# Optimization experiments

Measured on AMD Instinct MI355X. Metric: run time of the kernel, lower is better.

## Reference

```python
import jax, jax.numpy as jnp
import numpy as np

EPS = 1e-6
SINKHORN_ITERS = 8
TEMPERATURE = 1.0
B, N, D = 4, 8192, 512
E, OUT = 8, 512
H = 1


def setup_inputs() -> dict:
    key = jax.random.key(0)
    k1, k2, k3 = jax.random.split(key, 3)
    x = jax.random.normal(k1, (B, N, D), dtype=jnp.float32)
    gate_weight = jax.random.normal(k2, (H, D, E), dtype=jnp.float32)
    experts = jax.random.normal(k3, (E, D, OUT), dtype=jnp.float32) * 0.02
    return {"x": x, "gate_weight": gate_weight, "experts": experts}


def _sinkhorn(logits):
    # logits: (b, h, n, e). log(clamp(.,eps)) then alternating row/col log-normalization.
    t = jnp.log(jnp.clip(logits, EPS)) / TEMPERATURE
    for _ in range(SINKHORN_ITERS):
        t = t - jax.nn.logsumexp(t, axis=-2, keepdims=True)  # normalize over tokens n
        t = t - jax.nn.logsumexp(t, axis=-1, keepdims=True)  # normalize over experts e
    return jnp.exp(t)


def reference(x, gate_weight, experts):
    b, n, d = x.shape
    e = experts.shape[0]
    m = n // e  # tokens per expert
    xh = x[:, None, :, :]  # b 1 n d  (single-headed -> h=1)
    gate_logits = jnp.einsum('bhnd,hde->bhne', xh, gate_weight)
    gates = _sinkhorn(gate_logits)  # b h n e
    # topk over token dim n, per expert: move n to last axis for lax.top_k
    g_t = jnp.swapaxes(gates, -1, -2)  # b h e n
    vals, idx = jax.lax.top_k(g_t, m)  # (b h e m), (b h e m)
    gate_values = jnp.transpose(vals, (2, 0, 1, 3))[..., None]  # e b h m 1
    # gather routed tokens: routed[e,b,h,m,d] = x[b,h,idx[b,h,e,m],d]
    routed = jnp.take_along_axis(xh[:, :, None, :, :], idx[..., None], axis=3)  # b h e m d
    routed = jnp.transpose(routed, (2, 0, 1, 3, 4))  # e b h m d
    expert_w = experts[:, None, :, :]  # e h i o with h=1 (rearrange 'e i o -> e 1 i o')
    outputs = jnp.einsum('ebhmi,ehio->ebhmo', routed, expert_w)  # e b h m o
    outputs = outputs * gate_values
    # scatter back (set semantics, matching einx set_at)
    bh_idx = idx.reshape(b, 1, e * m)  # b h (e m)
    bh_vals = jnp.transpose(outputs, (1, 2, 0, 3, 4)).reshape(b, 1, e * m, outputs.shape[-1])
    def scat(i1, v1):
        return jnp.zeros((n, v1.shape[-1]), dtype=v1.dtype).at[i1].set(v1)
    routed_back = jax.vmap(jax.vmap(scat))(bh_idx, bh_vals)  # b h n o
    return routed_back[:, 0]  # b n o
```

## Files before the change

kernel.cpp:

```cpp
#include <hip/hip_runtime.h>
#include <hip/hip_bf16.h>

#define BB 4
#define NN 8192
#define DD 512
#define EE 8
#define OUTD 512
#define TOPM 1024
#define EPSV 1e-6f
#define ITERS 8

using s16x8 = __attribute__((ext_vector_type(8))) short;
using f32x4 = __attribute__((ext_vector_type(4))) float;
typedef unsigned long long u64;

__device__ __forceinline__ unsigned short f2bf(float f) {
  unsigned u = __float_as_uint(f);
  return (unsigned short)((u + 0x7FFFu + ((u >> 16) & 1u)) >> 16);
}

__device__ __forceinline__ void gll16(const void* g, void* l) {
  __builtin_amdgcn_global_load_lds((const __attribute__((address_space(1))) void*)g,
                                   (__attribute__((address_space(3))) void*)l, 16, 0, 0);
}

__global__ __launch_bounds__(256) void k_gate(const float* __restrict__ x,
                                              const float* __restrict__ gw,
                                              float* __restrict__ t0,
                                              unsigned short* __restrict__ xbf,
                                              int* __restrict__ eo,
                                              int* __restrict__ counts,
                                              const float* __restrict__ W,
                                              unsigned short* __restrict__ WT) {
  const int tid = threadIdx.x;
  if (blockIdx.x >= 2048) {
    __shared__ float tl[32][33];
    const int widx = blockIdx.x - 2048;
    const int e = widx >> 8, rem = widx & 255;
    const int k0 = (rem >> 4) * 32, n0 = (rem & 15) * 32;
    const int ty = tid >> 5, tx = tid & 31;
    const float* src = W + ((long)e * DD + k0) * OUTD + n0;
#pragma unroll
    for (int j = 0; j < 4; ++j)
      tl[ty + j * 8][tx] = src[(long)(ty + j * 8) * OUTD + tx];
    __syncthreads();
    unsigned short* dst = WT + ((long)e * OUTD + n0) * DD + k0;
#pragma unroll
    for (int j = 0; j < 4; ++j)
      dst[(long)(ty + j * 8) * DD + tx] = f2bf(tl[tx][ty + j * 8]);
    return;
  }
  if (tid < 16) eo[blockIdx.x * 16 + tid] = -1;
  if (blockIdx.x == 0 && tid >= 64 && tid < 64 + BB * EE) counts[tid - 64] = 0;
  const int lane = tid & 63;
  const int w    = tid >> 6;
  float gwf[64];
  const float* gb = gw + (lane * 8) * EE;
#pragma unroll
  for (int q = 0; q < 16; ++q) {
    float4 t = *(const float4*)(gb + q * 4);
    gwf[q * 4 + 0] = t.x; gwf[q * 4 + 1] = t.y;
    gwf[q * 4 + 2] = t.z; gwf[q * 4 + 3] = t.w;
  }
#pragma unroll
  for (int q = 0; q < 64; ++q) asm volatile("" : "+v"(gwf[q]));

  const long row0 = (long)blockIdx.x * 16 + w * 4;
  float4 xa[4], xb[4];
#pragma unroll
  for (int i = 0; i < 4; ++i) {
    const float* xr = x + (row0 + i) * DD + lane * 8;
    xa[i] = *(const float4*)(xr);
    xb[i] = *(const float4*)(xr + 4);
  }
  float vout[4];
#pragma unroll
  for (int i = 0; i < 4; ++i) {
    float xv[8] = {xa[i].x, xa[i].y, xa[i].z, xa[i].w,
                   xb[i].x, xb[i].y, xb[i].z, xb[i].w};
    s16x8 xo;
#pragma unroll
    for (int j = 0; j < 8; ++j) xo[j] = (short)f2bf(xv[j]);
    *(s16x8*)(xbf + (row0 + i) * DD + lane * 8) = xo;

    float acc[8] = {0.f,0.f,0.f,0.f,0.f,0.f,0.f,0.f};
#pragma unroll
    for (int q = 0; q < 8; ++q)
#pragma unroll
      for (int e = 0; e < 8; ++e) acc[e] += xv[q] * gwf[q * 8 + e];
    const bool o1 = lane & 1;
    float own, oth, b0, b1, b2, b3, c0, c1, v;
    own = o1 ? acc[1] : acc[0]; oth = o1 ? acc[0] : acc[1];
    b0 = own + __shfl_xor(oth, 1);
    own = o1 ? acc[3] : acc[2]; oth = o1 ? acc[2] : acc[3];
    b1 = own + __shfl_xor(oth, 1);
    own = o1 ? acc[5] : acc[4]; oth = o1 ? acc[4] : acc[5];
    b2 = own + __shfl_xor(oth, 1);
    own = o1 ? acc[7] : acc[6]; oth = o1 ? acc[6] : acc[7];
    b3 = own + __shfl_xor(oth, 1);
    const bool o2 = lane & 2;
    own = o2 ? b1 : b0; oth = o2 ? b0 : b1;
    c0 = own + __shfl_xor(oth, 2);
    own = o2 ? b3 : b2; oth = o2 ? b2 : b3;
    c1 = own + __shfl_xor(oth, 2);
    const bool o4 = lane & 4;
    own = o4 ? c1 : c0; oth = o4 ? c0 : c1;
    v = own + __shfl_xor(oth, 4);
    v += __shfl_xor(v, 8);
    v += __shfl_xor(v, 16);
    v += __shfl_xor(v, 32);
    vout[i] = v;
  }
  const int gsel = lane >> 3;
  float vsel = vout[0];
  vsel = (gsel == 1) ? vout[1] : vsel;
  vsel = (gsel == 2) ? vout[2] : vsel;
  vsel = (gsel == 3) ? vout[3] : vsel;
  if (lane < 32) t0[row0 * EE + lane] = logf(fmaxf(vsel, EPSV));
}

__global__ __launch_bounds__(1024) void k_sink5(const float* __restrict__ t0,
                                                float* __restrict__ R,
                                                float* __restrict__ C) {
  const int b = blockIdx.x;
  const int tid = threadIdx.x;
  const int wv = tid >> 6, ln = tid & 63;
  const float* tb = t0 + (long)b * NN * EE;
  float E[8][8], u[8], dl[8];
  __shared__ float ws[16][8];
  __shared__ float Csh[8];
  __shared__ float Ssh[8];
#pragma unroll
  for (int j = 0; j < 8; ++j) {
    const float* p = tb + (long)(j * 1024 + tid) * EE;
    float4 a = *(const float4*)p, b4 = *(const float4*)(p + 4);
    E[j][0] = expf(a.x);  E[j][1] = expf(a.y);
    E[j][2] = expf(a.z);  E[j][3] = expf(a.w);
    E[j][4] = expf(b4.x); E[j][5] = expf(b4.y);
    E[j][6] = expf(b4.z); E[j][7] = expf(b4.w);
    u[j] = 1.f;
  }
  for (int it = 0; it < ITERS; ++it) {
    float P[8] = {0.f,0.f,0.f,0.f,0.f,0.f,0.f,0.f};
#pragma unroll
    for (int j = 0; j < 8; ++j)
#pragma unroll
      for (int e = 0; e < 8; ++e) P[e] += E[j][e] * u[j];
#pragma unroll
    for (int d = 1; d <= 4; d <<= 1) {
#pragma unroll
      for (int e = 0; e < 8; ++e) {
        float tmp = __shfl_xor(P[e], d);
        P[e] += ((ln & d) == (e & d)) ? tmp : 0.f;
      }
    }
    float pv = P[0];
#pragma unroll
    for (int e = 1; e < 8; ++e) pv = ((ln & 7) == e) ? P[e] : pv;
#pragma unroll
    for (int d = 8; d < 64; d <<= 1) pv += __shfl_xor(pv, d);
    if (ln < 8) ws[wv][ln] = pv;
    __syncthreads();
    if (tid < 64) {
      const int q = ln >> 3, e = ln & 7;
      float s = ws[q][e] + ws[q + 8][e];
#pragma unroll
      for (int d = 8; d < 64; d <<= 1) s += __shfl_xor(s, d);
      if (ln < 8) { Csh[ln] = 1.f / s; Ssh[ln] = s; }
    }
    __syncthreads();
    float vv[8];
#pragma unroll
    for (int e = 0; e < 8; ++e) vv[e] = Csh[e];
#pragma unroll
    for (int j = 0; j < 8; ++j) {
      float d0 = E[j][0] * vv[0];
#pragma unroll
      for (int e = 1; e < 8; ++e) d0 += E[j][e] * vv[e];
      dl[j] = d0;
      u[j] = 1.f / d0;
    }
    __syncthreads();
  }
#pragma unroll
  for (int j = 0; j < 8; ++j) R[(long)b * NN + j * 1024 + tid] = logf(dl[j]);
  if (tid < 8) C[b * EE + tid] = logf(Ssh[tid]);
}

__global__ __launch_bounds__(1024) void k_topk(const float* __restrict__ t0,
                                               const float* __restrict__ R,
                                               int* __restrict__ expert_of) {
  __shared__ unsigned key[NN];
  __shared__ int hist[256];
  __shared__ int bcast[2];
  __shared__ int wsum[16];
  const int b = blockIdx.x >> 3, e = blockIdx.x & 7;
  const int tid = threadIdx.x;
  const int wv = tid >> 6, ln = tid & 63;
  const float* t = t0 + (long)b * NN * EE + e;
  const float* Rb = R + b * NN;
  if (tid < 256) hist[tid] = 0;
  __syncthreads();
  for (int n = tid; n < NN; n += 1024) {
    float f = t[n * EE] - Rb[n];
    unsigned u = __float_as_uint(f);
    u = (u & 0x80000000u) ? ~u : (u | 0x80000000u);
    key[n] = u;
    atomicAdd(&hist[u >> 24], 1);
  }
  __syncthreads();
  unsigned prefix = 0, mask = 0;
  int k = TOPM;
  for (int shift = 24; shift >= 0; shift -= 8) {
    if (tid < 64) {
      const int4 h4 = *(const int4*)&hist[ln * 4];
      const int r3 = h4.w, r2 = h4.z + r3, r1 = h4.y + r2, r0 = h4.x + r1;
      int suf = r0;
#pragma unroll
      for (int d = 1; d < 64; d <<= 1) {
        int o = __shfl_down(suf, d);
        if (ln + d < 64) suf += o;
      }
      const int above = suf - r0;
      const int cum0 = above + r0, cum1 = above + r1;
      const int cum2 = above + r2, cum3 = above + r3;
      if (cum0 >= k && cum1 < k) { bcast[0] = k - cum1; bcast[1] = ln * 4 + 0; }
      if (cum1 >= k && cum2 < k) { bcast[0] = k - cum2; bcast[1] = ln * 4 + 1; }
      if (cum2 >= k && cum3 < k) { bcast[0] = k - cum3; bcast[1] = ln * 4 + 2; }
      if (cum3 >= k && above < k) { bcast[0] = k - above; bcast[1] = ln * 4 + 3; }
    }
    __syncthreads();
    k = bcast[0];
    prefix |= ((unsigned)bcast[1]) << shift;
    mask |= (255u << shift);
    if (shift == 0) break;
    if (tid < 256) hist[tid] = 0;
    __syncthreads();
    const int nsh = shift - 8;
    for (int n = tid; n < NN; n += 1024) {
      unsigned u = key[n];
      if ((u & mask) == prefix) atomicAdd(&hist[(u >> nsh) & 255], 1);
    }
    __syncthreads();
  }
  const unsigned theta = prefix;
  const int need = k;
  const int base = tid * 8;
  int c = 0;
#pragma unroll
  for (int j = 0; j < 8; ++j) if (key[base + j] == theta) ++c;
  int inc = c;
#pragma unroll
  for (int d = 1; d < 64; d <<= 1) {
    int o = __shfl_up(inc, d);
    if (ln >= d) inc += o;
  }
  if (ln == 63) wsum[wv] = inc;
  __syncthreads();
  if (tid == 0) {
    int runv = 0;
    for (int i = 0; i < 16; ++i) { int t2 = wsum[i]; wsum[i] = runv; runv += t2; }
  }
  __syncthreads();
  int run = wsum[wv] + inc - c;
  int* eo = expert_of + b * NN;
  for (int j = 0; j < 8; ++j) {
    int n = base + j;
    unsigned u = key[n];
    bool sel = false;
    if (u > theta) sel = true;
    else if (u == theta) { if (run < need) sel = true; ++run; }
    if (sel) atomicMax(&eo[n], e);
  }
}

__global__ __launch_bounds__(256) void k_post(const int* __restrict__ expert_of,
                                              const float* __restrict__ t0,
                                              const float* __restrict__ R,
                                              const float* __restrict__ C,
                                              int* __restrict__ counts,
                                              int* __restrict__ lists,
                                              float* __restrict__ gvals,
                                              float* __restrict__ out) {
  const int tid = threadIdx.x;
  if (blockIdx.x >= 128) {
    const int row = (blockIdx.x - 128) * 4 + (tid >> 6);
    if (expert_of[row] >= 0) return;
    const int ln = tid & 63;
    float4 z = make_float4(0.f, 0.f, 0.f, 0.f);
    float4* p = (float4*)(out + (long)row * OUTD) + ln;
    p[0] = z; p[64] = z;
    return;
  }
  __shared__ int hist8[8], base8[8];
  if (tid < 8) hist8[tid] = 0;
  __syncthreads();
  const long i = (long)blockIdx.x * 256 + tid;
  const int b = (int)(i >> 13);
  const int e = expert_of[i];
  int lpos = -1;
  if (e >= 0) lpos = atomicAdd(&hist8[e], 1);
  __syncthreads();
  if (tid < 8 && hist8[tid] > 0)
    base8[tid] = atomicAdd(&counts[b * EE + tid], hist8[tid]);
  __syncthreads();
  if (e >= 0) {
    const int n = (int)(i & (NN - 1));
    const int be = b * EE + e;
    const int slot = be * TOPM + base8[e] + lpos;
    lists[slot] = n;
    gvals[slot] = expf(t0[i * EE + e] - C[be] - R[i]);
  }
}

__global__ __launch_bounds__(256) void k_gemm(const unsigned short* __restrict__ xbf,
                                              const unsigned short* __restrict__ WT,
                                              const int* __restrict__ counts,
                                              const int* __restrict__ lists,
                                              const float* __restrict__ gvals,
                                              float* __restrict__ out) {
  const int id = blockIdx.x;
  const int xq = id >> 8;
  const int be = (id >> 3) & 31;
  const int yq = id & 7;
  const int b = be >> 3, e = be & 7;
  const int cnt = counts[be];
  const int r0 = yq * 128;
  if (r0 >= cnt) return;
  const int c0 = xq * 128;

  __shared__ unsigned short As[128 * 64];
  __shared__ unsigned short Bs[128 * 64];
  __shared__ int   rowTok[128];
  __shared__ float rowG[128];

  const int tid = threadIdx.x;
  if (tid < 128) {
    int r = r0 + tid;
    rowTok[tid] = (r < cnt) ? lists[be * TOPM + r] : -1;
    rowG[tid]   = (r < cnt) ? gvals[be * TOPM + r] : 0.f;
  }
  __syncthreads();

  const int w = tid >> 6, l = tid & 63;
  const int rbase = w * 32 + (l >> 3);
  const int sL = l & 7;
  const unsigned short* xb_b = xbf + (long)b * NN * DD;
  const unsigned short* wt_e = WT + (long)e * OUTD * DD;
  int tokc[4]; int sGa[4], sGb[4];
#pragma unroll
  for (int c = 0; c < 4; ++c) {
    int r = rbase + c * 8;
    int tk = rowTok[r]; if (tk < 0) tk = 0;
    tokc[c] = tk;
    sGa[c] = (sL ^ (r & 7)) * 8;
    sGb[c] = sGa[c];
  }

  const int wr = w >> 1, wc = w & 1;
  const int fr = l & 15, fq = l >> 4;
  int aoff[4][2], boff[4][2];
#pragma unroll
  for (int m = 0; m < 4; ++m) {
#pragma unroll
    for (int kk = 0; kk < 2; ++kk) {
      int row = wr * 64 + m * 16 + fr;
      aoff[m][kk] = row * 64 + (((fq + 4 * kk) ^ (row & 7)) * 8);
      int col = wc * 64 + m * 16 + fr;
      boff[m][kk] = col * 64 + (((fq + 4 * kk) ^ (col & 7)) * 8);
    }
  }

  f32x4 acc[4][4] = {};

#define STAGE(kb) {                                                          \
    int ko = (kb) * 64;                                                      \
    _Pragma("unroll")                                                        \
    for (int c = 0; c < 4; ++c) {                                            \
      int r = rbase + c * 8;                                                 \
      gll16(xb_b + (long)tokc[c] * DD + ko + sGa[c],                         \
            As + (w * 32 + c * 8) * 64);                                     \
      gll16(wt_e + (long)(c0 + r) * DD + ko + sGb[c],                        \
            Bs + (w * 32 + c * 8) * 64);                                     \
    }                                                                        \
  }

  STAGE(0);
  for (int kb = 0; kb < 8; ++kb) {
    __syncthreads();
    s16x8 af[4][2], bf_[4][2];
#pragma unroll
    for (int m = 0; m < 4; ++m) {
      af[m][0] = *(const s16x8*)(As + aoff[m][0]);
      af[m][1] = *(const s16x8*)(As + aoff[m][1]);
      bf_[m][0] = *(const s16x8*)(Bs + boff[m][0]);
      bf_[m][1] = *(const s16x8*)(Bs + boff[m][1]);
    }
    __syncthreads();
    if (kb < 7) STAGE(kb + 1);
#pragma unroll
    for (int kk = 0; kk < 2; ++kk)
#pragma unroll
      for (int m = 0; m < 4; ++m)
#pragma unroll
        for (int n = 0; n < 4; ++n)
          acc[m][n] = __builtin_amdgcn_mfma_f32_16x16x32_bf16(af[m][kk], bf_[n][kk], acc[m][n], 0, 0, 0);
  }
#undef STAGE

#pragma unroll
  for (int m = 0; m < 4; ++m) {
    int rbase2 = wr * 64 + m * 16 + fq * 4;
    int tok[4]; float g[4];
#pragma unroll
    for (int j = 0; j < 4; ++j) { tok[j] = rowTok[rbase2 + j]; g[j] = rowG[rbase2 + j]; }
#pragma unroll
    for (int n = 0; n < 4; ++n) {
      int col = c0 + wc * 64 + n * 16 + fr;
#pragma unroll
      for (int j = 0; j < 4; ++j) {
        if (tok[j] >= 0)
          out[((long)b * NN + tok[j]) * OUTD + col] = acc[m][n][j] * g[j];
      }
    }
  }
}

extern "C" void kernel_launch(void* const* d_in, const int* in_sizes, int n_in,
                              void* d_out, int out_size, void* d_ws, size_t ws_size,
                              hipStream_t stream) {
  const float* x  = (const float*)d_in[0];
  const float* gw = (const float*)d_in[1];
  const float* ex = (const float*)d_in[2];
  float* out = (float*)d_out;

  char* wsb = (char*)d_ws;
  float*          t0     = (float*)(wsb);
  unsigned short* xbf    = (unsigned short*)(wsb + (1l << 20));
  unsigned short* WT     = (unsigned short*)(wsb + (33l << 20));
  const long base = 37l << 20;
  float*          R      = (float*)(wsb + base);
  int*            eo     = (int*)  (wsb + base + (128l << 10));
  int*            lists  = (int*)  (wsb + base + (256l << 10));
  float*          gvals  = (float*)(wsb + base + (384l << 10));
  float*          C      = (float*)(wsb + base + (512l << 10));
  int*            counts = (int*)  (wsb + base + (512l << 10) + 1024);

  k_gate<<<2048 + 2048, 256, 0, stream>>>(x, gw, t0, xbf, eo, counts, ex, WT);
  k_sink5<<<BB, 1024, 0, stream>>>(t0, R, C);
  k_topk<<<BB * EE, 1024, 0, stream>>>(t0, R, eo);
  k_post<<<128 + (BB * NN) / 4, 256, 0, stream>>>(eo, t0, R, C, counts, lists, gvals, out);
  k_gemm<<<1024, 256, 0, stream>>>(xbf, WT, counts, lists, gvals, out);
}
```

Before: 107.0 us.

## Fuse Sinkhorn normalization into top-k kernel with redundant per-expert recompute

Merges the Sinkhorn kernel into the top-k kernel. Each of the 32 blocks (batch × expert) redundantly recomputes the 8-iteration Sinkhorn for its batch and builds radix-select keys directly from registers, with only the e==0 block writing R and C for later kernels. This removes one kernel launch and the global round-trip of R between the two kernels, and spreads Sinkhorn over more CUs, at the cost of eight times the redundant Sinkhorn arithmetic and higher register and LDS pressure per block.

```diff
diff --git a/kernel.cpp b/kernel.cpp
--- a/kernel.cpp
+++ b/kernel.cpp
@@ -119,17 +119,21 @@
   if (lane < 32) t0[row0 * EE + lane] = logf(fmaxf(vsel, EPSV));
 }
 
-__global__ __launch_bounds__(1024) void k_sink5(const float* __restrict__ t0,
-                                                float* __restrict__ R,
-                                                float* __restrict__ C) {
-  const int b = blockIdx.x;
+__global__ __launch_bounds__(1024) void k_topk(const float* __restrict__ t0,
+                                               float* __restrict__ R,
+                                               float* __restrict__ C,
+                                               int* __restrict__ expert_of) {
+  __shared__ unsigned key[NN];
+  __shared__ int hist[256];
+  __shared__ int bcast[2];
+  __shared__ int wsum[16];
+  __shared__ float ws[16][8], Csh[8], Ssh[8];
+  const int b = blockIdx.x >> 3, e = blockIdx.x & 7;
   const int tid = threadIdx.x;
   const int wv = tid >> 6, ln = tid & 63;
   const float* tb = t0 + (long)b * NN * EE;
-  float E[8][8], u[8], dl[8];
-  __shared__ float ws[16][8];
-  __shared__ float Csh[8];
-  __shared__ float Ssh[8];
+
+  float E[8][8], u[8], dl[8], tvm[8];
 #pragma unroll
   for (int j = 0; j < 8; ++j) {
     const float* p = tb + (long)(j * 1024 + tid) * EE;
@@ -138,6 +142,7 @@
     E[j][2] = expf(a.z);  E[j][3] = expf(a.w);
     E[j][4] = expf(b4.x); E[j][5] = expf(b4.y);
     E[j][6] = expf(b4.z); E[j][7] = expf(b4.w);
+    tvm[j] = p[e];
     u[j] = 1.f;
   }
   for (int it = 0; it < ITERS; ++it) {
@@ -145,25 +150,25 @@
 #pragma unroll
     for (int j = 0; j < 8; ++j)
 #pragma unroll
-      for (int e = 0; e < 8; ++e) P[e] += E[j][e] * u[j];
+      for (int e2 = 0; e2 < 8; ++e2) P[e2] += E[j][e2] * u[j];
 #pragma unroll
     for (int d = 1; d <= 4; d <<= 1) {
 #pragma unroll
-      for (int e = 0; e < 8; ++e) {
-        float tmp = __shfl_xor(P[e], d);
-        P[e] += ((ln & d) == (e & d)) ? tmp : 0.f;
+      for (int e2 = 0; e2 < 8; ++e2) {
+        float tmp = __shfl_xor(P[e2], d);
+        P[e2] += ((ln & d) == (e2 & d)) ? tmp : 0.f;
       }
     }
     float pv = P[0];
 #pragma unroll
-    for (int e = 1; e < 8; ++e) pv = ((ln & 7) == e) ? P[e] : pv;
+    for (int e2 = 1; e2 < 8; ++e2) pv = ((ln & 7) == e2) ? P[e2] : pv;
 #pragma unroll
     for (int d = 8; d < 64; d <<= 1) pv += __shfl_xor(pv, d);
     if (ln < 8) ws[wv][ln] = pv;
     __syncthreads();
     if (tid < 64) {
-      const int q = ln >> 3, e = ln & 7;
-      float s = ws[q][e] + ws[q + 8][e];
+      const int q = ln >> 3, e2 = ln & 7;
+      float s = ws[q][e2] + ws[q + 8][e2];
 #pragma unroll
       for (int d = 8; d < 64; d <<= 1) s += __shfl_xor(s, d);
       if (ln < 8) { Csh[ln] = 1.f / s; Ssh[ln] = s; }
@@ -171,42 +176,33 @@
     __syncthreads();
     float vv[8];
 #pragma unroll
-    for (int e = 0; e < 8; ++e) vv[e] = Csh[e];
+    for (int e2 = 0; e2 < 8; ++e2) vv[e2] = Csh[e2];
 #pragma unroll
     for (int j = 0; j < 8; ++j) {
       float d0 = E[j][0] * vv[0];
 #pragma unroll
-      for (int e = 1; e < 8; ++e) d0 += E[j][e] * vv[e];
+      for (int e2 = 1; e2 < 8; ++e2) d0 += E[j][e2] * vv[e2];
       dl[j] = d0;
       u[j] = 1.f / d0;
     }
     __syncthreads();
   }
-#pragma unroll
-  for (int j = 0; j < 8; ++j) R[(long)b * NN + j * 1024 + tid] = logf(dl[j]);
-  if (tid < 8) C[b * EE + tid] = logf(Ssh[tid]);
-}
-
-__global__ __launch_bounds__(1024) void k_topk(const float* __restrict__ t0,
-                                               const float* __restrict__ R,
-                                               int* __restrict__ expert_of) {
-  __shared__ unsigned key[NN];
-  __shared__ int hist[256];
-  __shared__ int bcast[2];
-  __shared__ int wsum[16];
-  const int b = blockIdx.x >> 3, e = blockIdx.x & 7;
-  const int tid = threadIdx.x;
-  const int wv = tid >> 6, ln = tid & 63;
-  const float* t = t0 + (long)b * NN * EE + e;
-  const float* Rb = R + b * NN;
+  if (e == 0) {
+#pragma unroll
+    for (int j = 0; j < 8; ++j) R[(long)b * NN + j * 1024 + tid] = logf(dl[j]);
+    if (tid < 8) C[b * EE + tid] = logf(Ssh[tid]);
+  }
+
   if (tid < 256) hist[tid] = 0;
   __syncthreads();
-  for (int n = tid; n < NN; n += 1024) {
-    float f = t[n * EE] - Rb[n];
-    unsigned u = __float_as_uint(f);
-    u = (u & 0x80000000u) ? ~u : (u | 0x80000000u);
-    key[n] = u;
-    atomicAdd(&hist[u >> 24], 1);
+#pragma unroll
+  for (int j = 0; j < 8; ++j) {
+    const int n = j * 1024 + tid;
+    float f = tvm[j] - logf(dl[j]);
+    unsigned uk = __float_as_uint(f);
+    uk = (uk & 0x80000000u) ? ~uk : (uk | 0x80000000u);
+    key[n] = uk;
+    atomicAdd(&hist[uk >> 24], 1);
   }
   __syncthreads();
   unsigned prefix = 0, mask = 0;
@@ -238,8 +234,8 @@
     __syncthreads();
     const int nsh = shift - 8;
     for (int n = tid; n < NN; n += 1024) {
-      unsigned u = key[n];
-      if ((u & mask) == prefix) atomicAdd(&hist[(u >> nsh) & 255], 1);
+      unsigned uk = key[n];
+      if ((uk & mask) == prefix) atomicAdd(&hist[(uk >> nsh) & 255], 1);
     }
     __syncthreads();
   }
@@ -266,10 +262,10 @@
   int* eo = expert_of + b * NN;
   for (int j = 0; j < 8; ++j) {
     int n = base + j;
-    unsigned u = key[n];
+    unsigned uk = key[n];
     bool sel = false;
-    if (u > theta) sel = true;
-    else if (u == theta) { if (run < need) sel = true; ++run; }
+    if (uk > theta) sel = true;
+    else if (uk == theta) { if (run < need) sel = true; ++run; }
     if (sel) atomicMax(&eo[n], e);
   }
 }
@@ -447,8 +443,7 @@
   int*            counts = (int*)  (wsb + base + (512l << 10) + 1024);
 
   k_gate<<<2048 + 2048, 256, 0, stream>>>(x, gw, t0, xbf, eo, counts, ex, WT);
-  k_sink5<<<BB, 1024, 0, stream>>>(t0, R, C);
-  k_topk<<<BB * EE, 1024, 0, stream>>>(t0, R, eo);
+  k_topk<<<BB * EE, 1024, 0, stream>>>(t0, R, C, eo);
   k_post<<<128 + (BB * NN) / 4, 256, 0, stream>>>(eo, t0, R, C, counts, lists, gvals, out);
   k_gemm<<<1024, 256, 0, stream>>>(xbf, WT, counts, lists, gvals, out);
 }
```

Measured after the change: 106.4 us. No clear change (-0.6%).
